# Performance work log

Hardware: AMD Instinct MI355X
Metric: run time of the kernel (lower is better)

The kernel has to match this reference:

```python
import jax, jax.numpy as jnp
import numpy as np

B, C, H, W = 4, 32, 512, 960

def _splat_one(inp, flow):
    # inp: [C+1, H, W] (features weighted by exp(metric), plus exp(metric) channel)
    # flow: [2, H, W]
    Cp = inp.shape[0]
    ox = jnp.arange(W, dtype=flow.dtype)[None, :] + flow[0]   # [H, W]
    oy = jnp.arange(H, dtype=flow.dtype)[:, None] + flow[1]   # [H, W]
    x0 = jnp.floor(ox).astype(jnp.int32)
    y0 = jnp.floor(oy).astype(jnp.int32)
    x1, y1 = x0 + 1, y0 + 1
    fx, fy = ox - x0, oy - y0
    corners = [
        (x0, y0, (1 - fx) * (1 - fy)),
        (x1, y0, fx * (1 - fy)),
        (x0, y1, (1 - fx) * fy),
        (x1, y1, fx * fy),
    ]
    flat = inp.reshape(Cp, H * W)
    acc = jnp.zeros((Cp, H * W), dtype=inp.dtype)
    for cx, cy, w in corners:
        valid = (cx >= 0) & (cx < W) & (cy >= 0) & (cy < H)
        idx = jnp.where(valid, cy * W + cx, 0).reshape(-1)
        wv = jnp.where(valid, w, 0.0).reshape(-1)
        acc = acc.at[:, idx].add(flat * wv[None, :])
    return acc.reshape(Cp, H, W)

def softmax_splatting(ten_input, ten_flow, ten_metric):
    # 'softmax' type: splat [input*exp(m), exp(m)], then normalize by last channel.
    em = jnp.exp(ten_metric)                      # [B,1,H,W]
    packed = jnp.concatenate([ten_input * em, em], axis=1)  # [B,C+1,H,W]
    out = jax.vmap(_splat_one)(packed, ten_flow)  # [B,C+1,H,W]
    num, den = out[:, :-1], out[:, -1:]
    den = jnp.where(den == 0.0, 1.0, den)
    return num / den

def setup_inputs() -> dict:
    key = jax.random.key(0)
    k1, k2, k3 = jax.random.split(key, 3)
    ten_input = jax.random.normal(k1, (B, C, H, W), dtype=jnp.float32)
    # SCALE=20 for pwcnet flows -> multi-pixel irregular displacements
    ten_flow = jax.random.normal(k2, (B, 2, H, W), dtype=jnp.float32) * 20.0
    ten_metric = jax.random.normal(k3, (B, 1, H, W), dtype=jnp.float32)
    beta = jnp.full((1,), -1.0, dtype=jnp.float32)  # nn.Parameter([-1])
    return {"ten_input": ten_input, "ten_flow": ten_flow, "ten_metric": ten_metric, "beta": beta}

def reference(ten_input, ten_flow, ten_metric, beta):
    return softmax_splatting(ten_input, ten_flow, beta.reshape(1, 1, 1, 1) * ten_metric)
```

## Files before the change

### kernel.cpp

```cpp
#include <hip/hip_runtime.h>

#define BB 4
#define CC 32
#define HH 512
#define WW 960
#define HWSZ (HH * WW)
#define NPIX (BB * HWSZ)
#define CS 36

__global__ __launch_bounds__(512) void splat_soa(
    const float* __restrict__ inp, const float* __restrict__ flow,
    const float* __restrict__ metric, const float* __restrict__ beta,
    float* __restrict__ acc)
{
    int t   = blockIdx.x * 512 + threadIdx.x;
    int c   = t & 31;
    int pix = t >> 5;
    int b   = pix / HWSZ;
    int rem = pix - b * HWSZ;
    int y   = rem / WW;
    int x   = rem - y * WW;

    float flx = flow[(size_t)b * 2 * HWSZ + rem];
    float fly = flow[(size_t)b * 2 * HWSZ + HWSZ + rem];
    float m   = metric[(size_t)b * HWSZ + rem];
    float em  = expf(beta[0] * m);

    float ox = (float)x + flx;
    float oy = (float)y + fly;
    float x0f = floorf(ox), y0f = floorf(oy);
    int   x0 = (int)x0f,   y0 = (int)y0f;
    int   x1 = x0 + 1,     y1 = y0 + 1;
    float fx = ox - x0f,   fy = oy - y0f;
    float gx = 1.0f - fx,  gy = 1.0f - fy;

    float val = inp[((size_t)b * CC + c) * HWSZ + rem] * em;
    float* ab = acc + (size_t)b * HWSZ * CS;

#define DO_CORNER(CX, CY, WGT)                                        \
    if ((unsigned)(CX) < (unsigned)WW && (unsigned)(CY) < (unsigned)HH) { \
        float* p = ab + ((size_t)(CY) * WW + (CX)) * CS;              \
        atomicAdd(p + c, val * (WGT));                                \
        if (c == 0) atomicAdd(p + 32, em * (WGT));                    \
    }
    DO_CORNER(x0, y0, gx * gy)
    DO_CORNER(x1, y0, fx * gy)
    DO_CORNER(x0, y1, gx * fy)
    DO_CORNER(x1, y1, fx * fy)
#undef DO_CORNER
}

__global__ __launch_bounds__(256) void norm_soa(
    const float* __restrict__ acc, float* __restrict__ out)
{
    int pix = blockIdx.x * 256 + threadIdx.x;
    if (pix >= NPIX) return;
    int b   = pix / HWSZ;
    int rem = pix - b * HWSZ;

    const float4* p = (const float4*)(acc + (size_t)pix * CS);
    float4 v[9];
#pragma unroll
    for (int i = 0; i < 9; ++i) v[i] = p[i];
    float den = v[8].x;
    if (den == 0.0f) den = 1.0f;

    const float* vf = (const float*)v;
    float* ob = out + (size_t)b * CC * HWSZ + rem;
#pragma unroll
    for (int c = 0; c < CC; ++c)
        ob[(size_t)c * HWSZ] = vf[c] / den;
}

__global__ __launch_bounds__(512) void splat_planar(
    const float* __restrict__ inp, const float* __restrict__ flow,
    const float* __restrict__ metric, const float* __restrict__ beta,
    float* __restrict__ out, float* __restrict__ den)
{
    int t   = blockIdx.x * 512 + threadIdx.x;
    int c   = t & 31;
    int pix = t >> 5;
    int b   = pix / HWSZ;
    int rem = pix - b * HWSZ;
    int y   = rem / WW;
    int x   = rem - y * WW;

    float flx = flow[(size_t)b * 2 * HWSZ + rem];
    float fly = flow[(size_t)b * 2 * HWSZ + HWSZ + rem];
    float m   = metric[(size_t)b * HWSZ + rem];
    float em  = expf(beta[0] * m);

    float ox = (float)x + flx;
    float oy = (float)y + fly;
    float x0f = floorf(ox), y0f = floorf(oy);
    int   x0 = (int)x0f,   y0 = (int)y0f;
    int   x1 = x0 + 1,     y1 = y0 + 1;
    float fx = ox - x0f,   fy = oy - y0f;
    float gx = 1.0f - fx,  gy = 1.0f - fy;

    float val = inp[((size_t)b * CC + c) * HWSZ + rem] * em;

#define DO_CORNER(CX, CY, WGT)                                        \
    if ((unsigned)(CX) < (unsigned)WW && (unsigned)(CY) < (unsigned)HH) { \
        size_t ti = (size_t)(CY) * WW + (CX);                         \
        atomicAdd(out + ((size_t)b * CC + c) * HWSZ + ti, val * (WGT)); \
        if (c == 0) atomicAdd(den + (size_t)b * HWSZ + ti, em * (WGT)); \
    }
    DO_CORNER(x0, y0, gx * gy)
    DO_CORNER(x1, y0, fx * gy)
    DO_CORNER(x0, y1, gx * fy)
    DO_CORNER(x1, y1, fx * fy)
#undef DO_CORNER
}

__global__ __launch_bounds__(256) void norm_planar(
    float* __restrict__ out, const float* __restrict__ den)
{
    int pix = blockIdx.x * 256 + threadIdx.x;
    if (pix >= NPIX) return;
    int b   = pix / HWSZ;
    int rem = pix - b * HWSZ;
    float d = den[pix];
    if (d == 0.0f) d = 1.0f;
    float* ob = out + (size_t)b * CC * HWSZ + rem;
#pragma unroll
    for (int c = 0; c < CC; ++c)
        ob[(size_t)c * HWSZ] /= d;
}

extern "C" void kernel_launch(void* const* d_in, const int* in_sizes, int n_in,
                              void* d_out, int out_size, void* d_ws, size_t ws_size,
                              hipStream_t stream) {
    const float* inp    = (const float*)d_in[0];
    const float* flow   = (const float*)d_in[1];
    const float* metric = (const float*)d_in[2];
    const float* beta   = (const float*)d_in[3];
    float* out = (float*)d_out;

    const size_t need = (size_t)NPIX * CS * sizeof(float);

    if (ws_size >= need) {
        hipMemsetAsync(d_ws, 0, need, stream);
        splat_soa<<<NPIX / 16, 512, 0, stream>>>(inp, flow, metric, beta,
                                                 (float*)d_ws);
        norm_soa<<<(NPIX + 255) / 256, 256, 0, stream>>>((const float*)d_ws, out);
    } else {
        hipMemsetAsync(d_out, 0, (size_t)NPIX * CC * sizeof(float), stream);
        hipMemsetAsync(d_ws, 0, (size_t)NPIX * sizeof(float), stream);
        splat_planar<<<NPIX / 16, 512, 0, stream>>>(inp, flow, metric, beta,
                                                    out, (float*)d_ws);
        norm_planar<<<(NPIX + 255) / 256, 256, 0, stream>>>(out, (const float*)d_ws);
    }
}
```

Measured before the change: 1.814 ms.

## Use persistent grid-stride splat with prefetch and split num/den accumulators

Measured after the change: 1.635 ms. 1.11x faster.

```diff
diff --git a/kernel.cpp b/kernel.cpp
--- a/kernel.cpp
+++ b/kernel.cpp
@@ -6,70 +6,92 @@
 #define WW 960
 #define HWSZ (HH * WW)
 #define NPIX (BB * HWSZ)
-#define CS 36
 
-__global__ __launch_bounds__(512) void splat_soa(
+#define NSLOT 16384
+#define ITERS (NPIX / NSLOT)
+
+__global__ __launch_bounds__(512) void splat2(
     const float* __restrict__ inp, const float* __restrict__ flow,
     const float* __restrict__ metric, const float* __restrict__ beta,
-    float* __restrict__ acc)
+    float* __restrict__ num, float* __restrict__ den)
 {
-    int t   = blockIdx.x * 512 + threadIdx.x;
-    int c   = t & 31;
-    int pix = t >> 5;
+    const float bta = beta[0];
+    int t    = blockIdx.x * 512 + threadIdx.x;
+    int c    = t & 31;
+    int slot = t >> 5;
+
+    int pix = slot;
     int b   = pix / HWSZ;
     int rem = pix - b * HWSZ;
-    int y   = rem / WW;
-    int x   = rem - y * WW;
-
     float flx = flow[(size_t)b * 2 * HWSZ + rem];
     float fly = flow[(size_t)b * 2 * HWSZ + HWSZ + rem];
     float m   = metric[(size_t)b * HWSZ + rem];
-    float em  = expf(beta[0] * m);
+    float vin = inp[((size_t)b * CC + c) * HWSZ + rem];
 
-    float ox = (float)x + flx;
-    float oy = (float)y + fly;
-    float x0f = floorf(ox), y0f = floorf(oy);
-    int   x0 = (int)x0f,   y0 = (int)y0f;
-    int   x1 = x0 + 1,     y1 = y0 + 1;
-    float fx = ox - x0f,   fy = oy - y0f;
-    float gx = 1.0f - fx,  gy = 1.0f - fy;
+    for (int it = 0; it < ITERS; ++it) {
+        float cflx = flx, cfly = fly, cm = m, cvin = vin;
+        int cpix = pix, cb = b, crem = rem;
 
-    float val = inp[((size_t)b * CC + c) * HWSZ + rem] * em;
-    float* ab = acc + (size_t)b * HWSZ * CS;
+        pix = cpix + NSLOT;
+        if (it + 1 < ITERS) {
+            b   = pix / HWSZ;
+            rem = pix - b * HWSZ;
+            flx = flow[(size_t)b * 2 * HWSZ + rem];
+            fly = flow[(size_t)b * 2 * HWSZ + HWSZ + rem];
+            m   = metric[(size_t)b * HWSZ + rem];
+            vin = inp[((size_t)b * CC + c) * HWSZ + rem];
+        }
 
-#define DO_CORNER(CX, CY, WGT)                                        \
-    if ((unsigned)(CX) < (unsigned)WW && (unsigned)(CY) < (unsigned)HH) { \
-        float* p = ab + ((size_t)(CY) * WW + (CX)) * CS;              \
-        atomicAdd(p + c, val * (WGT));                                \
-        if (c == 0) atomicAdd(p + 32, em * (WGT));                    \
+        int y = crem / WW;
+        int x = crem - y * WW;
+        float em = expf(bta * cm);
+        float ox = (float)x + cflx;
+        float oy = (float)y + cfly;
+        float x0f = floorf(ox), y0f = floorf(oy);
+        int   x0 = (int)x0f,   y0 = (int)y0f;
+        int   x1 = x0 + 1,     y1 = y0 + 1;
+        float fx = ox - x0f,   fy = oy - y0f;
+        float gx = 1.0f - fx,  gy = 1.0f - fy;
+
+        float val = cvin * em;
+        size_t base = (size_t)cb * HWSZ;
+
+#define DO_CORNER(CX, CY, WGT)                                            \
+        if ((unsigned)(CX) < (unsigned)WW && (unsigned)(CY) < (unsigned)HH) { \
+            size_t ti = base + (size_t)(CY) * WW + (CX);                  \
+            atomicAdd(num + ti * CC + c, val * (WGT));                    \
+            if (c == 0) atomicAdd(den + ti, em * (WGT));                  \
+        }
+        DO_CORNER(x0, y0, gx * gy)
+        DO_CORNER(x1, y0, fx * gy)
+        DO_CORNER(x0, y1, gx * fy)
+        DO_CORNER(x1, y1, fx * fy)
+#undef DO_CORNER
     }
-    DO_CORNER(x0, y0, gx * gy)
-    DO_CORNER(x1, y0, fx * gy)
-    DO_CORNER(x0, y1, gx * fy)
-    DO_CORNER(x1, y1, fx * fy)
-#undef DO_CORNER
 }
 
-__global__ __launch_bounds__(256) void norm_soa(
-    const float* __restrict__ acc, float* __restrict__ out)
+__global__ __launch_bounds__(256) void norm2(
+    const float* __restrict__ num, const float* __restrict__ den,
+    float* __restrict__ out)
 {
     int pix = blockIdx.x * 256 + threadIdx.x;
     if (pix >= NPIX) return;
     int b   = pix / HWSZ;
     int rem = pix - b * HWSZ;
 
-    const float4* p = (const float4*)(acc + (size_t)pix * CS);
-    float4 v[9];
+    const float4* p = (const float4*)(num + (size_t)pix * CC);
+    float4 v[8];
 #pragma unroll
-    for (int i = 0; i < 9; ++i) v[i] = p[i];
-    float den = v[8].x;
-    if (den == 0.0f) den = 1.0f;
+    for (int i = 0; i < 8; ++i) v[i] = p[i];
+    float d = den[pix];
+    if (d == 0.0f) d = 1.0f;
+    float inv = 1.0f / d;
 
     const float* vf = (const float*)v;
     float* ob = out + (size_t)b * CC * HWSZ + rem;
 #pragma unroll
     for (int c = 0; c < CC; ++c)
-        ob[(size_t)c * HWSZ] = vf[c] / den;
+        ob[(size_t)c * HWSZ] = vf[c] * inv;
 }
 
 __global__ __launch_bounds__(512) void splat_planar(
@@ -137,18 +159,22 @@
     const float* beta   = (const float*)d_in[3];
     float* out = (float*)d_out;
 
-    const size_t need = (size_t)NPIX * CS * sizeof(float);
+    const size_t num_bytes = (size_t)NPIX * CC * sizeof(float);
+    const size_t den_bytes = (size_t)NPIX * sizeof(float);
+    const size_t need = num_bytes + den_bytes;
 
     if (ws_size >= need) {
+        float* num = (float*)d_ws;
+        float* den = (float*)((char*)d_ws + num_bytes);
         hipMemsetAsync(d_ws, 0, need, stream);
-        splat_soa<<<NPIX / 16, 512, 0, stream>>>(inp, flow, metric, beta,
-                                                 (float*)d_ws);
-        norm_soa<<<(NPIX + 255) / 256, 256, 0, stream>>>((const float*)d_ws, out);
+        splat2<<<NSLOT * 32 / 512, 512, 0, stream>>>(inp, flow, metric, beta,
+                                                     num, den);
+        norm2<<<NPIX / 256, 256, 0, stream>>>(num, den, out);
     } else {
         hipMemsetAsync(d_out, 0, (size_t)NPIX * CC * sizeof(float), stream);
         hipMemsetAsync(d_ws, 0, (size_t)NPIX * sizeof(float), stream);
         splat_planar<<<NPIX / 16, 512, 0, stream>>>(inp, flow, metric, beta,
                                                     out, (float*)d_ws);
-        norm_planar<<<(NPIX + 255) / 256, 256, 0, stream>>>(out, (const float*)d_ws);
+        norm_planar<<<NPIX / 256, 256, 0, stream>>>(out, (const float*)d_ws);
     }
 }
```
